# Performance work log

Measured on AMD Instinct MI355X. Metric: run time of the kernel, lower is better.

Reference implementation:

```python
import jax, jax.numpy as jnp
import numpy as np

DIM = 1024
NUM_HEADS = 16
HEAD_DIM = DIM // NUM_HEADS
SCALE = HEAD_DIM ** -0.5


def setup_inputs() -> dict:
    key = jax.random.key(0)
    ks = jax.random.split(key, 12)
    B, N, M, C = 4, 512, 2048, DIM
    x = jax.random.normal(ks[0], (B, N, C), dtype=jnp.float32)
    context = jax.random.normal(ks[1], (B, M, C), dtype=jnp.float32)
    mask = jax.random.randint(ks[2], (B, M), 0, 2, dtype=jnp.int32)
    mask = mask.at[:, 0].set(1)  # ensure at least one valid key per row
    w = 0.02
    Wq = jax.random.normal(ks[3], (C, C), dtype=jnp.float32) * w
    bq = jnp.zeros((C,), dtype=jnp.float32)
    Wk = jax.random.normal(ks[4], (C, C), dtype=jnp.float32) * w
    bk = jnp.zeros((C,), dtype=jnp.float32)
    Wv = jax.random.normal(ks[5], (C, C), dtype=jnp.float32) * w
    bv = jnp.zeros((C,), dtype=jnp.float32)
    Wo = jax.random.normal(ks[6], (C, C), dtype=jnp.float32) * w
    bo = jnp.zeros((C,), dtype=jnp.float32)
    return {"x": x, "context": context, "ctx_key_padding_mask": mask,
            "Wq": Wq, "bq": bq, "Wk": Wk, "bk": bk,
            "Wv": Wv, "bv": bv, "Wo": Wo, "bo": bo}


def reference(x, context, ctx_key_padding_mask, Wq, bq, Wk, bk, Wv, bv, Wo, bo):
    B, N, C = x.shape
    M = context.shape[1]
    H, D = NUM_HEADS, HEAD_DIM
    # torch nn.Linear: y = x @ W.T + b
    q = (x @ Wq.T + bq).reshape(B, N, H, D)
    k = (context @ Wk.T + bk).reshape(B, M, H, D)
    v = (context @ Wv.T + bv).reshape(B, M, H, D)
    scores = jnp.einsum('bnhd,bmhd->bhnm', q, k) * SCALE  # [B,H,N,M]
    neg = jnp.finfo(scores.dtype).min
    bias = jnp.where(ctx_key_padding_mask[:, None, None, :] != 0, 0.0, neg).astype(scores.dtype)
    attn = jax.nn.softmax(scores + bias, axis=-1)
    out = jnp.einsum('bhnm,bmhd->bnhd', attn, v).reshape(B, N, C)
    return out @ Wo.T + bo
```

## Files before the change

### kernel.cpp

```cpp
#include <hip/hip_runtime.h>
#include <hip/hip_bf16.h>
#include <stdint.h>


typedef __attribute__((ext_vector_type(4))) float f32x4;
typedef __attribute__((ext_vector_type(8))) __bf16 bf16x8;
typedef __attribute__((ext_vector_type(8))) unsigned short u16x8;

#define DEVI __device__ __forceinline__

#define QSC (0.125f * 1.44269504088896f)

DEVI f32x4 mfma16(u16x8 a, u16x8 b, f32x4 c) {
  return __builtin_amdgcn_mfma_f32_16x16x32_bf16(
      __builtin_bit_cast(bf16x8, a), __builtin_bit_cast(bf16x8, b), c, 0, 0, 0);
}

DEVI unsigned short f2bf(float f) {
  union { float f; unsigned int u; } x; x.f = f;
  unsigned int u = x.u;
  return (unsigned short)((u + 0x7fffu + ((u >> 16) & 1u)) >> 16);
}

DEVI float exp2_fast(float x) {
#if __has_builtin(__builtin_amdgcn_exp2f)
  return __builtin_amdgcn_exp2f(x);
#else
  return exp2f(x);
#endif
}

DEVI void llds16(const void* g, void* l) {
  __builtin_amdgcn_global_load_lds(
      (const __attribute__((address_space(1))) void*)g,
      (__attribute__((address_space(3))) void*)l, 16, 0, 0);
}

__global__ __launch_bounds__(256)
void cast_fused(const float* __restrict__ x, const float* __restrict__ ctx,
                const float* __restrict__ wq, const float* __restrict__ wk,
                const float* __restrict__ wv, const float* __restrict__ wo,
                unsigned short* __restrict__ xb, unsigned short* __restrict__ cb,
                unsigned short* __restrict__ wqb, unsigned short* __restrict__ wkb,
                unsigned short* __restrict__ wvb, unsigned short* __restrict__ wob) {
  int bid = blockIdx.x;
  const float* src; unsigned short* dst; float scale = 1.f;
  if (bid < 2048)        { src = x;   dst = xb; }
  else if (bid < 10240)  { src = ctx; dst = cb;  bid -= 2048; }
  else if (bid < 11264)  { src = wq;  dst = wqb; bid -= 10240; scale = QSC; }
  else if (bid < 12288)  { src = wk;  dst = wkb; bid -= 11264; }
  else if (bid < 13312)  { src = wv;  dst = wvb; bid -= 12288; }
  else                   { src = wo;  dst = wob; bid -= 13312; }
  int idx = (bid * 256 + threadIdx.x) * 4;
  const float4 v = *(const float4*)(src + idx);
  ushort4 o;
  o.x = f2bf(v.x * scale); o.y = f2bf(v.y * scale);
  o.z = f2bf(v.z * scale); o.w = f2bf(v.w * scale);
  *(ushort4*)(dst + idx) = o;
}

DEVI void epi_store(f32x4 (&acc)[4][4], const float* __restrict__ bias,
                    float bscale, void* __restrict__ Cout,
                    int bm, int bn, int logS, int mode,
                    unsigned short* cst, int tid, int wave, int l15, int quad) {
  const int wm = wave & 1, wn = wave >> 1;
  __syncthreads();
  for (int half = 0; half < 2; ++half) {
    if (wm == half) {
#pragma unroll
      for (int mi = 0; mi < 4; ++mi)
#pragma unroll
        for (int ni = 0; ni < 4; ++ni)
#pragma unroll
          for (int r = 0; r < 4; ++r) {
            int lrow = mi * 16 + quad * 4 + r;
            int lcol = wn * 64 + ni * 16 + l15;
            unsigned short bv = f2bf(acc[mi][ni][r] + bias[bn + lcol] * bscale);
            if (mode == 0) cst[lrow * 136 + lcol] = bv;
            else           cst[lcol * 72 + lrow] = bv;
          }
    }
    __syncthreads();
    if (mode == 0) {
      int lrow = tid >> 2, cc = (tid & 3) * 32;
      int row = bm + half * 64 + lrow;
      int S = 1 << logS;
      int b = row >> logS, sl = row & (S - 1);
#pragma unroll
      for (int j = 0; j < 4; ++j) {
        int col = bn + cc + j * 8;
        int h = col >> 6, d8 = (col & 63) >> 3;
        size_t base = (((size_t)(b * 16 + h)) << logS) * 64 +
                      (size_t)(sl >> 4) * 1024 + d8 * 128 + (sl & 15) * 8;
        *(u16x8*)&((unsigned short*)Cout)[base] =
            *(const u16x8*)&cst[lrow * 136 + cc + j * 8];
      }
    } else {
      int c = tid >> 1, rc = (tid & 1) * 32;
      int gc = bn + c, h = gc >> 6, d = gc & 63;
      int b = bm >> 11;
#pragma unroll
      for (int j = 0; j < 4; ++j) {
        int key = (bm & 2047) + half * 64 + rc + j * 8;
        size_t base = (size_t)(b * 16 + h) * 131072 +
                      (size_t)(((key >> 6) * 4 + (d >> 4)) * 8 + ((key >> 3) & 7)) * 128 +
                      (d & 15) * 8;
        *(u16x8*)&((unsigned short*)Cout)[base] =
            *(const u16x8*)&cst[c * 72 + rc + j * 8];
      }
    }
    __syncthreads();
  }
}

DEVI void kv_body(const unsigned short* __restrict__ A,
                  const unsigned short* __restrict__ WK,
                  const unsigned short* __restrict__ WV,
                  const float* __restrict__ bk, const float* __restrict__ bv,
                  unsigned short* __restrict__ kh, unsigned short* __restrict__ vt,
                  int bm, int bn, unsigned short* sh) {
  constexpr int K = 1024;
  unsigned short* As = sh;
  unsigned short* Ks = sh + 128 * 64;
  unsigned short* Vs = sh + 2 * 128 * 64;

  const int tid = threadIdx.x;
  const int wave = tid >> 6, lane = tid & 63;
  const int l15 = lane & 15, quad = lane >> 4;
  const int wm = wave & 1, wn = wave >> 1;

  f32x4 ak[4][4] = {}, av[4][4] = {};

  for (int k0 = 0; k0 < K; k0 += 64) {
    __syncthreads();
#pragma unroll
    for (int c = 0; c < 4; ++c) {
      int s = c * 256 + tid;
      int m = s >> 3;
      int k8 = (s & 7) ^ (m & 7);
      llds16(A + (size_t)(bm + m) * K + k0 + k8 * 8, &As[s * 8]);
      llds16(WK + (size_t)(bn + m) * K + k0 + k8 * 8, &Ks[s * 8]);
      llds16(WV + (size_t)(bn + m) * K + k0 + k8 * 8, &Vs[s * 8]);
    }
    __syncthreads();
#pragma unroll
    for (int ks = 0; ks < 2; ++ks) {
      const int k8 = ks * 4 + quad;
      u16x8 af[4], bf[4];
#pragma unroll
      for (int i = 0; i < 4; ++i) {
        int m = wm * 64 + i * 16 + l15;
        af[i] = *(const u16x8*)(&As[(m * 8 + (k8 ^ (m & 7))) * 8]);
      }
#pragma unroll
      for (int i = 0; i < 4; ++i) {
        int n = wn * 64 + i * 16 + l15;
        bf[i] = *(const u16x8*)(&Ks[(n * 8 + (k8 ^ (n & 7))) * 8]);
      }
#pragma unroll
      for (int mi = 0; mi < 4; ++mi)
#pragma unroll
        for (int ni = 0; ni < 4; ++ni)
          ak[mi][ni] = mfma16(af[mi], bf[ni], ak[mi][ni]);
#pragma unroll
      for (int i = 0; i < 4; ++i) {
        int n = wn * 64 + i * 16 + l15;
        bf[i] = *(const u16x8*)(&Vs[(n * 8 + (k8 ^ (n & 7))) * 8]);
      }
#pragma unroll
      for (int mi = 0; mi < 4; ++mi)
#pragma unroll
        for (int ni = 0; ni < 4; ++ni)
          av[mi][ni] = mfma16(af[mi], bf[ni], av[mi][ni]);
    }
  }

  epi_store(ak, bk, 1.f, kh, bm, bn, 11, 0, sh, tid, wave, l15, quad);
  epi_store(av, bv, 1.f, vt, bm, bn, 11, 2, sh, tid, wave, l15, quad);
}

DEVI void q_body(const unsigned short* __restrict__ A,
                 const unsigned short* __restrict__ W,
                 const float* __restrict__ bias,
                 unsigned short* __restrict__ Cout,
                 int bm, int bn, unsigned short* sh) {
  constexpr int K = 1024;
  unsigned short* As = sh;
  unsigned short* Bs = sh + 128 * 64;

  const int tid = threadIdx.x;
  const int wave = tid >> 6, lane = tid & 63;
  const int l15 = lane & 15, quad = lane >> 4;
  const int wm = wave & 1, wn = wave >> 1;

  f32x4 acc[4][4] = {};

  for (int k0 = 0; k0 < K; k0 += 64) {
    __syncthreads();
#pragma unroll
    for (int c = 0; c < 4; ++c) {
      int s = c * 256 + tid;
      int m = s >> 3;
      int k8 = (s & 7) ^ (m & 7);
      llds16(A + (size_t)(bm + m) * K + k0 + k8 * 8, &As[s * 8]);
      llds16(W + (size_t)(bn + m) * K + k0 + k8 * 8, &Bs[s * 8]);
    }
    __syncthreads();
#pragma unroll
    for (int ks = 0; ks < 2; ++ks) {
      const int k8 = ks * 4 + quad;
      u16x8 af[4], bf[4];
#pragma unroll
      for (int i = 0; i < 4; ++i) {
        int m = wm * 64 + i * 16 + l15;
        af[i] = *(const u16x8*)(&As[(m * 8 + (k8 ^ (m & 7))) * 8]);
        int n = wn * 64 + i * 16 + l15;
        bf[i] = *(const u16x8*)(&Bs[(n * 8 + (k8 ^ (n & 7))) * 8]);
      }
#pragma unroll
      for (int mi = 0; mi < 4; ++mi)
#pragma unroll
        for (int ni = 0; ni < 4; ++ni)
          acc[mi][ni] = mfma16(af[mi], bf[ni], acc[mi][ni]);
    }
  }

  epi_store(acc, bias, QSC, Cout, bm, bn, 9, 0, sh, tid, wave, l15, quad);
}

__global__ __launch_bounds__(256, 2)
void gemm_qkv(const unsigned short* __restrict__ xb,
              const unsigned short* __restrict__ cb,
              const unsigned short* __restrict__ wq,
              const unsigned short* __restrict__ wk,
              const unsigned short* __restrict__ wv,
              const float* __restrict__ bq, const float* __restrict__ bk,
              const float* __restrict__ bv,
              unsigned short* __restrict__ qh, unsigned short* __restrict__ kh,
              unsigned short* __restrict__ vt) {
  __shared__ __align__(16) unsigned short sh[128 * 64 * 3];
  const int x = blockIdx.x, y = blockIdx.y;
  if (y < 8) {
    kv_body(cb, wk, wv, bk, bv, kh, vt, x * 128, y * 128, sh);
  } else {
    q_body(xb, wq, bq, qh, (x & 15) * 128, (y - 8) * 512 + (x >> 4) * 128, sh);
  }
}

__global__ __launch_bounds__(256)
void gemm_o(const unsigned short* __restrict__ A,
            const unsigned short* __restrict__ W,
            const float* __restrict__ bo, float* __restrict__ out) {
  constexpr int K = 1024;
  __shared__ __align__(16) unsigned short As[64 * 64];
  __shared__ __align__(16) unsigned short Bs[128 * 64];

  const int tid = threadIdx.x;
  const int wave = tid >> 6, lane = tid & 63;
  const int l15 = lane & 15, quad = lane >> 4;
  const int bm = blockIdx.x * 64, bn = blockIdx.y * 128;

  f32x4 acc[4][2] = {};

  for (int k0 = 0; k0 < K; k0 += 64) {
    __syncthreads();
#pragma unroll
    for (int c = 0; c < 2; ++c) {
      int s = c * 256 + tid;
      int m = s >> 3, k8 = (s & 7) ^ (m & 7);
      llds16(A + (size_t)(bm + m) * K + k0 + k8 * 8, &As[s * 8]);
    }
#pragma unroll
    for (int c = 0; c < 4; ++c) {
      int s = c * 256 + tid;
      int m = s >> 3, k8 = (s & 7) ^ (m & 7);
      llds16(W + (size_t)(bn + m) * K + k0 + k8 * 8, &Bs[s * 8]);
    }
    __syncthreads();
#pragma unroll
    for (int ks = 0; ks < 2; ++ks) {
      const int k8 = ks * 4 + quad;
      u16x8 af[4], bf[2];
#pragma unroll
      for (int i = 0; i < 4; ++i) {
        int m = i * 16 + l15;
        af[i] = *(const u16x8*)(&As[(m * 8 + (k8 ^ (m & 7))) * 8]);
      }
#pragma unroll
      for (int i = 0; i < 2; ++i) {
        int n = wave * 32 + i * 16 + l15;
        bf[i] = *(const u16x8*)(&Bs[(n * 8 + (k8 ^ (n & 7))) * 8]);
      }
#pragma unroll
      for (int mi = 0; mi < 4; ++mi)
#pragma unroll
        for (int ni = 0; ni < 2; ++ni)
          acc[mi][ni] = mfma16(af[mi], bf[ni], acc[mi][ni]);
    }
  }

#pragma unroll
  for (int mi = 0; mi < 4; ++mi)
#pragma unroll
    for (int ni = 0; ni < 2; ++ni)
#pragma unroll
      for (int r = 0; r < 4; ++r) {
        int row = bm + mi * 16 + quad * 4 + r;
        int col = bn + wave * 32 + ni * 16 + l15;
        out[(size_t)row * 1024 + col] = acc[mi][ni][r] + bo[col];
      }
}

#define PS 72
__global__ __launch_bounds__(256, 1)
void attn_kernel(const unsigned short* __restrict__ Q,
                 const unsigned short* __restrict__ K,
                 const unsigned short* __restrict__ Vt,
                 const int* __restrict__ mask,
                 unsigned short* __restrict__ O) {
  __shared__ float bias_lds[2048];
  __shared__ __align__(16) unsigned short p_lds[4][2][16 * PS];
  __shared__ float l_lds[4][64];
  __shared__ __align__(16) float o_comb[64][68];

  const int tid = threadIdx.x;
  const int wave = tid >> 6, lane = tid & 63;
  const int l15 = lane & 15, quad = lane >> 4;
  const int bh = blockIdx.x, b = bh >> 4, h = bh & 15;
  const int q0 = blockIdx.y * 64;

  {
    const int* mb = mask + b * 2048;
    for (int i = tid; i < 2048; i += 256)
      bias_lds[i] = mb[i] ? -8.f : -1e30f;
  }
  __syncthreads();

  const unsigned short* Qb = Q + (size_t)bh * 32768 + (size_t)(q0 >> 4) * 1024;
  const unsigned short* Kb = K + (size_t)bh * 131072;
  const unsigned short* Vb = Vt + (size_t)bh * 131072;

  u16x8 aq[4][2];
#pragma unroll
  for (int qg = 0; qg < 4; ++qg)
#pragma unroll
    for (int ks = 0; ks < 2; ++ks)
      aq[qg][ks] = *(const u16x8*)(Qb + ((qg * 8 + ks * 4 + quad) * 16 + l15) * 8);

  f32x4 o_acc[4][4] = {};
  float l_s[4] = {0.f, 0.f, 0.f, 0.f};

  u16x8 kf[2][4];

  auto load_k = [&](int kb) {
    const int kg0 = kb >> 4;
#pragma unroll
    for (int ns = 0; ns < 4; ++ns)
#pragma unroll
      for (int ks = 0; ks < 2; ++ks)
        kf[ks][ns] = *(const u16x8*)(Kb + (((size_t)(kg0 + ns) * 8 + ks * 4 + quad) * 16 + l15) * 8);
  };

  load_k(wave * 64);

#pragma unroll 1
  for (int t = 0; t < 8; ++t) {
    const int kb = wave * 64 + t * 256;
    const int kb_next = kb + (t < 7 ? 256 : 0);

    u16x8 vf[2][4];
    const int kt4 = (kb >> 6) * 4;
#pragma unroll
    for (int nd = 0; nd < 4; ++nd)
#pragma unroll
      for (int ks = 0; ks < 2; ++ks)
        vf[ks][nd] = *(const u16x8*)(Vb + (((size_t)(kt4 + nd) * 8 + ks * 4 + quad) * 16 + l15) * 8);
    f32x4 bfr[4];
#pragma unroll
    for (int ns = 0; ns < 4; ++ns)
      bfr[ns] = *(const f32x4*)&bias_lds[kb + ns * 16 + quad * 4];

#pragma unroll
    for (int qg = 0; qg < 4; ++qg) {
      f32x4 sfr[4];
#pragma unroll
      for (int ns = 0; ns < 4; ++ns) {
        f32x4 sa = bfr[ns];
#pragma unroll
        for (int ks = 0; ks < 2; ++ks)
          sa = mfma16(kf[ks][ns], aq[qg][ks], sa);
        sfr[ns] = sa;
      }

      if (qg == 3) load_k(kb_next);

      float rsum = 0.f;
#pragma unroll
      for (int ns = 0; ns < 4; ++ns) {
        unsigned int pr[4];
#pragma unroll
        for (int r = 0; r < 4; ++r) {
          float p = exp2_fast(sfr[ns][r]);
          unsigned int u = __builtin_bit_cast(unsigned int, p) & 0xffff0000u;
          rsum += __builtin_bit_cast(float, u);
          pr[r] = u;
        }
        uint2 pw;
        pw.x = __builtin_amdgcn_perm(pr[1], pr[0], 0x07060302u);
        pw.y = __builtin_amdgcn_perm(pr[3], pr[2], 0x07060302u);
        *(uint2*)&p_lds[wave][qg & 1][l15 * PS + ns * 16 + quad * 4] = pw;
      }
      rsum += __shfl_xor(rsum, 16, 64);
      rsum += __shfl_xor(rsum, 32, 64);
      l_s[qg] += rsum;

#pragma unroll
      for (int ks = 0; ks < 2; ++ks) {
        u16x8 pf = *(const u16x8*)&p_lds[wave][qg & 1][l15 * PS + ks * 32 + quad * 8];
#pragma unroll
        for (int nd = 0; nd < 4; ++nd)
          o_acc[qg][nd] = mfma16(pf, vf[ks][nd], o_acc[qg][nd]);
      }
    }
  }

  if (quad == 0) {
#pragma unroll
    for (int qg = 0; qg < 4; ++qg)
      l_lds[wave][qg * 16 + l15] = l_s[qg];
  }
  __syncthreads();

  for (int w = 0; w < 4; ++w) {
    if (wave == w) {
#pragma unroll
      for (int qg = 0; qg < 4; ++qg)
#pragma unroll
        for (int r = 0; r < 4; ++r) {
          const int q = qg * 16 + quad * 4 + r;
#pragma unroll
          for (int nd = 0; nd < 4; ++nd) {
            const int d = nd * 16 + l15;
            float v = o_acc[qg][nd][r];
            if (w == 0) o_comb[q][d] = v;
            else        o_comb[q][d] += v;
          }
        }
    }
    __syncthreads();
  }

  {
    const int q = tid >> 2, dc = (tid & 3) * 16;
    const float inv = 1.f / (l_lds[0][q] + l_lds[1][q] + l_lds[2][q] + l_lds[3][q]);
    unsigned short* Ob = O + ((size_t)(b * 512 + q0 + q)) * 1024 + h * 64 + dc;
    u16x8 o1, o2;
#pragma unroll
    for (int j = 0; j < 8; ++j) o1[j] = f2bf(o_comb[q][dc + j] * inv);
#pragma unroll
    for (int j = 0; j < 8; ++j) o2[j] = f2bf(o_comb[q][dc + 8 + j] * inv);
    *(u16x8*)(Ob) = o1;
    *(u16x8*)(Ob + 8) = o2;
  }
}

extern "C" void kernel_launch(void* const* d_in, const int* in_sizes, int n_in,
                              void* d_out, int out_size, void* d_ws, size_t ws_size,
                              hipStream_t stream) {
  const float* x   = (const float*)d_in[0];
  const float* ctx = (const float*)d_in[1];
  const int* mask  = (const int*)d_in[2];
  const float* Wq  = (const float*)d_in[3];
  const float* bq  = (const float*)d_in[4];
  const float* Wk  = (const float*)d_in[5];
  const float* bk  = (const float*)d_in[6];
  const float* Wv  = (const float*)d_in[7];
  const float* bv  = (const float*)d_in[8];
  const float* Wo  = (const float*)d_in[9];
  const float* bo  = (const float*)d_in[10];

  char* ws = (char*)d_ws;
  unsigned short* xb  = (unsigned short*)(ws + ((size_t)0  << 20));
  unsigned short* cb  = (unsigned short*)(ws + ((size_t)4  << 20));
  unsigned short* wqb = (unsigned short*)(ws + ((size_t)20 << 20));
  unsigned short* wkb = (unsigned short*)(ws + ((size_t)22 << 20));
  unsigned short* wvb = (unsigned short*)(ws + ((size_t)24 << 20));
  unsigned short* wob = (unsigned short*)(ws + ((size_t)26 << 20));
  unsigned short* qh  = (unsigned short*)(ws + ((size_t)28 << 20));
  unsigned short* kh  = (unsigned short*)(ws + ((size_t)32 << 20));
  unsigned short* vt  = (unsigned short*)(ws + ((size_t)48 << 20));
  unsigned short* ah  = (unsigned short*)(ws + ((size_t)64 << 20));

  cast_fused<<<14336, 256, 0, stream>>>(x, ctx, Wq, Wk, Wv, Wo,
                                        xb, cb, wqb, wkb, wvb, wob);
  gemm_qkv<<<dim3(64, 10), 256, 0, stream>>>(xb, cb, wqb, wkb, wvb,
                                             bq, bk, bv, qh, kh, vt);
  attn_kernel<<<dim3(64, 8), 256, 0, stream>>>(qh, kh, vt, mask, ah);
  gemm_o<<<dim3(32, 8), 256, 0, stream>>>(ah, wob, bo, (float*)d_out);
}
```

Measured before the change: 212.0 us.

## Compact unmasked context rows and skip padded keys in KV projection and attention

After: 204.5 us. 1.04x faster.

```diff
diff --git a/kernel.cpp b/kernel.cpp
--- a/kernel.cpp
+++ b/kernel.cpp
@@ -37,26 +37,70 @@
 }
 
 __global__ __launch_bounds__(256)
+void compact_mask(const int* __restrict__ mask, int* __restrict__ cnt,
+                  int* __restrict__ idx) {
+  __shared__ int psum[256];
+  const int b = blockIdx.x, tid = threadIdx.x;
+  const int* mb = mask + b * 2048;
+  int v[8], s = 0;
+#pragma unroll
+  for (int j = 0; j < 8; ++j) { v[j] = (mb[tid * 8 + j] != 0); s += v[j]; }
+  psum[tid] = s;
+  __syncthreads();
+  for (int off = 1; off < 256; off <<= 1) {
+    int t = (tid >= off) ? psum[tid - off] : 0;
+    __syncthreads();
+    psum[tid] += t;
+    __syncthreads();
+  }
+  int base = tid ? psum[tid - 1] : 0;
+#pragma unroll
+  for (int j = 0; j < 8; ++j)
+    if (v[j]) { idx[b * 2048 + base] = tid * 8 + j; ++base; }
+  if (tid == 255) cnt[b] = psum[255];
+}
+
+__global__ __launch_bounds__(256)
 void cast_fused(const float* __restrict__ x, const float* __restrict__ ctx,
                 const float* __restrict__ wq, const float* __restrict__ wk,
                 const float* __restrict__ wv, const float* __restrict__ wo,
+                const int* __restrict__ cnt, const int* __restrict__ idx,
                 unsigned short* __restrict__ xb, unsigned short* __restrict__ cb,
                 unsigned short* __restrict__ wqb, unsigned short* __restrict__ wkb,
                 unsigned short* __restrict__ wvb, unsigned short* __restrict__ wob) {
   int bid = blockIdx.x;
+  const int tid = threadIdx.x;
+  if (bid >= 2048 && bid < 10240) {
+    int r = bid - 2048;
+    int b = r >> 11, j = r & 2047;
+    int c = cnt[b];
+    unsigned short* dst = cb + (size_t)r * 1024 + tid * 4;
+    if (j >= c) {
+      if (j < ((c + 255) & ~255)) {
+        ushort4 z; z.x = z.y = z.z = z.w = 0;
+        *(ushort4*)dst = z;
+      }
+      return;
+    }
+    const float* src = ctx + ((size_t)(b * 2048 + idx[b * 2048 + j])) * 1024 + tid * 4;
+    const float4 v = *(const float4*)src;
+    ushort4 o;
+    o.x = f2bf(v.x); o.y = f2bf(v.y); o.z = f2bf(v.z); o.w = f2bf(v.w);
+    *(ushort4*)dst = o;
+    return;
+  }
   const float* src; unsigned short* dst; float scale = 1.f;
   if (bid < 2048)        { src = x;   dst = xb; }
-  else if (bid < 10240)  { src = ctx; dst = cb;  bid -= 2048; }
   else if (bid < 11264)  { src = wq;  dst = wqb; bid -= 10240; scale = QSC; }
   else if (bid < 12288)  { src = wk;  dst = wkb; bid -= 11264; }
   else if (bid < 13312)  { src = wv;  dst = wvb; bid -= 12288; }
   else                   { src = wo;  dst = wob; bid -= 13312; }
-  int idx = (bid * 256 + threadIdx.x) * 4;
-  const float4 v = *(const float4*)(src + idx);
+  int e = (bid * 256 + tid) * 4;
+  const float4 v = *(const float4*)(src + e);
   ushort4 o;
   o.x = f2bf(v.x * scale); o.y = f2bf(v.y * scale);
   o.z = f2bf(v.z * scale); o.w = f2bf(v.w * scale);
-  *(ushort4*)(dst + idx) = o;
+  *(ushort4*)(dst + e) = o;
 }
 
 DEVI void epi_store(f32x4 (&acc)[4][4], const float* __restrict__ bias,
@@ -236,12 +280,16 @@
               const unsigned short* __restrict__ wv,
               const float* __restrict__ bq, const float* __restrict__ bk,
               const float* __restrict__ bv,
+              const int* __restrict__ cnt,
               unsigned short* __restrict__ qh, unsigned short* __restrict__ kh,
               unsigned short* __restrict__ vt) {
   __shared__ __align__(16) unsigned short sh[128 * 64 * 3];
   const int x = blockIdx.x, y = blockIdx.y;
   if (y < 8) {
-    kv_body(cb, wk, wv, bk, bv, kh, vt, x * 128, y * 128, sh);
+    const int bm = x * 128;
+    const int cpad = (cnt[bm >> 11] + 255) & ~255;
+    if ((bm & 2047) >= cpad) return;
+    kv_body(cb, wk, wv, bk, bv, kh, vt, bm, y * 128, sh);
   } else {
     q_body(xb, wq, bq, qh, (x & 15) * 128, (y - 8) * 512 + (x >> 4) * 128, sh);
   }
@@ -316,7 +364,7 @@
 void attn_kernel(const unsigned short* __restrict__ Q,
                  const unsigned short* __restrict__ K,
                  const unsigned short* __restrict__ Vt,
-                 const int* __restrict__ mask,
+                 const int* __restrict__ cnt,
                  unsigned short* __restrict__ O) {
   __shared__ float bias_lds[2048];
   __shared__ __align__(16) unsigned short p_lds[4][2][16 * PS];
@@ -329,11 +377,11 @@
   const int bh = blockIdx.x, b = bh >> 4, h = bh & 15;
   const int q0 = blockIdx.y * 64;
 
-  {
-    const int* mb = mask + b * 2048;
-    for (int i = tid; i < 2048; i += 256)
-      bias_lds[i] = mb[i] ? -8.f : -1e30f;
-  }
+  const int c = cnt[b];
+  const int T = (c + 255) >> 8;
+
+  for (int i = tid; i < 2048; i += 256)
+    bias_lds[i] = (i < c) ? -8.f : -1e30f;
   __syncthreads();
 
   const unsigned short* Qb = Q + (size_t)bh * 32768 + (size_t)(q0 >> 4) * 1024;
@@ -364,9 +412,9 @@
   load_k(wave * 64);
 
 #pragma unroll 1
-  for (int t = 0; t < 8; ++t) {
+  for (int t = 0; t < T; ++t) {
     const int kb = wave * 64 + t * 256;
-    const int kb_next = kb + (t < 7 ? 256 : 0);
+    const int kb_next = kb + (t + 1 < T ? 256 : 0);
 
     u16x8 vf[2][4];
     const int kt4 = (kb >> 6) * 4;
@@ -490,11 +538,14 @@
   unsigned short* kh  = (unsigned short*)(ws + ((size_t)32 << 20));
   unsigned short* vt  = (unsigned short*)(ws + ((size_t)48 << 20));
   unsigned short* ah  = (unsigned short*)(ws + ((size_t)64 << 20));
-
-  cast_fused<<<14336, 256, 0, stream>>>(x, ctx, Wq, Wk, Wv, Wo,
+  int* cnt = (int*)d_out;
+  int* idx = (int*)d_out + 4;
+
+  compact_mask<<<4, 256, 0, stream>>>(mask, cnt, idx);
+  cast_fused<<<14336, 256, 0, stream>>>(x, ctx, Wq, Wk, Wv, Wo, cnt, idx,
                                         xb, cb, wqb, wkb, wvb, wob);
   gemm_qkv<<<dim3(64, 10), 256, 0, stream>>>(xb, cb, wqb, wkb, wvb,
-                                             bq, bk, bv, qh, kh, vt);
-  attn_kernel<<<dim3(64, 8), 256, 0, stream>>>(qh, kh, vt, mask, ah);
+                                             bq, bk, bv, cnt, qh, kh, vt);
+  attn_kernel<<<dim3(64, 8), 256, 0, stream>>>(qh, kh, vt, cnt, ah);
   gemm_o<<<dim3(32, 8), 256, 0, stream>>>(ah, wob, bo, (float*)d_out);
 }
```

## Compact unmasked context rows and skip padded keys in KV projection and attention

Applied to the files above, without the earlier changes.

Result: faster. 190.5 us (-10.1%).

```diff
diff --git a/kernel.cpp b/kernel.cpp
--- a/kernel.cpp
+++ b/kernel.cpp
@@ -40,23 +40,64 @@
 void cast_fused(const float* __restrict__ x, const float* __restrict__ ctx,
                 const float* __restrict__ wq, const float* __restrict__ wk,
                 const float* __restrict__ wv, const float* __restrict__ wo,
+                const int* __restrict__ mask,
                 unsigned short* __restrict__ xb, unsigned short* __restrict__ cb,
                 unsigned short* __restrict__ wqb, unsigned short* __restrict__ wkb,
                 unsigned short* __restrict__ wvb, unsigned short* __restrict__ wob) {
   int bid = blockIdx.x;
+  const int tid = threadIdx.x;
+  if (bid >= 2048 && bid < 10240) {
+    __shared__ int red[256][2];
+    int r = bid - 2048;
+    int b = r >> 11, i = r & 2047;
+    const int* mb = mask + b * 2048;
+    int sall = 0, spre = 0;
+#pragma unroll
+    for (int j = 0; j < 8; ++j) {
+      int p = tid * 8 + j;
+      int v = (mb[p] != 0);
+      sall += v;
+      spre += (p < i) ? v : 0;
+    }
+    red[tid][0] = spre; red[tid][1] = sall;
+    __syncthreads();
+    for (int off = 128; off > 0; off >>= 1) {
+      if (tid < off) { red[tid][0] += red[tid + off][0]; red[tid][1] += red[tid + off][1]; }
+      __syncthreads();
+    }
+    const int pre = red[0][0], c = red[0][1];
+    const int valid = (mb[i] != 0);
+    int dst;
+    if (valid) {
+      dst = pre;
+    } else {
+      dst = c + (i - pre);
+      if (dst >= ((c + 255) & ~255)) return;
+    }
+    unsigned short* dp = cb + ((size_t)(b * 2048 + dst)) * 1024 + tid * 4;
+    if (valid) {
+      const float4 v = *(const float4*)(ctx + ((size_t)(b * 2048 + i)) * 1024 + tid * 4);
+      ushort4 o;
+      o.x = f2bf(v.x); o.y = f2bf(v.y); o.z = f2bf(v.z); o.w = f2bf(v.w);
+      *(ushort4*)dp = o;
+    } else {
+      ushort4 z; z.x = z.y = z.z = z.w = 0;
+      *(ushort4*)dp = z;
+    }
+    return;
+  }
   const float* src; unsigned short* dst; float scale = 1.f;
   if (bid < 2048)        { src = x;   dst = xb; }
-  else if (bid < 10240)  { src = ctx; dst = cb;  bid -= 2048; }
   else if (bid < 11264)  { src = wq;  dst = wqb; bid -= 10240; scale = QSC; }
   else if (bid < 12288)  { src = wk;  dst = wkb; bid -= 11264; }
   else if (bid < 13312)  { src = wv;  dst = wvb; bid -= 12288; }
   else                   { src = wo;  dst = wob; bid -= 13312; }
-  int idx = (bid * 256 + threadIdx.x) * 4;
-  const float4 v = *(const float4*)(src + idx);
+  int e = (bid * 256 + tid) * 4;
+  const float4 v = *(const float4*)(src + e);
   ushort4 o;
   o.x = f2bf(v.x * scale); o.y = f2bf(v.y * scale);
   o.z = f2bf(v.z * scale); o.w = f2bf(v.w * scale);
-  *(ushort4*)(dst + idx) = o;
+  *(ushort4*)(dst + e) = o;
 }
 
 DEVI void epi_store(f32x4 (&acc)[4][4], const float* __restrict__ bias,
@@ -236,14 +277,42 @@
               const unsigned short* __restrict__ wv,
               const float* __restrict__ bq, const float* __restrict__ bk,
               const float* __restrict__ bv,
+              const int* __restrict__ mask,
               unsigned short* __restrict__ qh, unsigned short* __restrict__ kh,
               unsigned short* __restrict__ vt) {
   __shared__ __align__(16) unsigned short sh[128 * 64 * 3];
-  const int x = blockIdx.x, y = blockIdx.y;
-  if (y < 8) {
-    kv_body(cb, wk, wv, bk, bv, kh, vt, x * 128, y * 128, sh);
-  } else {
-    q_body(xb, wq, bq, qh, (x & 15) * 128, (y - 8) * 512 + (x >> 4) * 128, sh);
+  __shared__ int qsum[260];
+  const int id = blockIdx.x;
+  const int tid = threadIdx.x;
+
+  {
+    int s = 0;
+    const int* mp = mask + tid * 32;
+#pragma unroll 8
+    for (int j = 0; j < 32; ++j) s += (mp[j] != 0);
+    qsum[tid] = s;
+    __syncthreads();
+    if (tid < 4) {
+      int tot = 0;
+      for (int k = 0; k < 64; ++k) tot += qsum[tid * 64 + k];
+      qsum[256 + tid] = tot;
+    }
+    __syncthreads();
+  }
+  const int nb0 = ((qsum[256] + 255) & ~255) >> 7;
+  const int nb1 = ((qsum[257] + 255) & ~255) >> 7;
+  const int nb2 = ((qsum[258] + 255) & ~255) >> 7;
+  const int nb3 = ((qsum[259] + 255) & ~255) >> 7;
+  const int L = nb0 + nb1 + nb2 + nb3;
+  if (id < L * 8) {
+    int xl = id >> 3, y = id & 7, b = 0;
+    if (xl >= nb0) { xl -= nb0; b = 1;
+      if (xl >= nb1) { xl -= nb1; b = 2;
+        if (xl >= nb2) { xl -= nb2; b = 3; } } }
+    kv_body(cb, wk, wv, bk, bv, kh, vt, b * 2048 + xl * 128, y * 128, sh);
+  } else if (id < L * 8 + 128) {
+    const int q = id - L * 8;
+    q_body(xb, wq, bq, qh, (q & 15) * 128, (q >> 4) * 128, sh);
   }
 }
 
@@ -312,16 +381,16 @@
 }
 
 #define PS 72
-__global__ __launch_bounds__(256, 1)
+__global__ __launch_bounds__(256, 2)
 void attn_kernel(const unsigned short* __restrict__ Q,
                  const unsigned short* __restrict__ K,
                  const unsigned short* __restrict__ Vt,
                  const int* __restrict__ mask,
                  unsigned short* __restrict__ O) {
-  __shared__ float bias_lds[2048];
   __shared__ __align__(16) unsigned short p_lds[4][2][16 * PS];
   __shared__ float l_lds[4][64];
   __shared__ __align__(16) float o_comb[64][68];
+  __shared__ int wsum[4];
 
   const int tid = threadIdx.x;
   const int wave = tid >> 6, lane = tid & 63;
@@ -331,10 +400,16 @@
 
   {
     const int* mb = mask + b * 2048;
-    for (int i = tid; i < 2048; i += 256)
-      bias_lds[i] = mb[i] ? -8.f : -1e30f;
-  }
-  __syncthreads();
+    int s = 0;
+#pragma unroll
+    for (int j = 0; j < 8; ++j) s += (mb[tid * 8 + j] != 0);
+#pragma unroll
+    for (int off = 1; off < 64; off <<= 1) s += __shfl_xor(s, off, 64);
+    if (lane == 0) wsum[wave] = s;
+    __syncthreads();
+  }
+  const int c = wsum[0] + wsum[1] + wsum[2] + wsum[3];
+  const int T = (c + 255) >> 8;
 
   const unsigned short* Qb = Q + (size_t)bh * 32768 + (size_t)(q0 >> 4) * 1024;
   const unsigned short* Kb = K + (size_t)bh * 131072;
@@ -364,9 +439,9 @@
   load_k(wave * 64);
 
 #pragma unroll 1
-  for (int t = 0; t < 8; ++t) {
+  for (int t = 0; t < T; ++t) {
     const int kb = wave * 64 + t * 256;
-    const int kb_next = kb + (t < 7 ? 256 : 0);
+    const int kb_next = kb + (t + 1 < T ? 256 : 0);
 
     u16x8 vf[2][4];
     const int kt4 = (kb >> 6) * 4;
@@ -375,10 +450,19 @@
 #pragma unroll
       for (int ks = 0; ks < 2; ++ks)
         vf[ks][nd] = *(const u16x8*)(Vb + (((size_t)(kt4 + nd) * 8 + ks * 4 + quad) * 16 + l15) * 8);
+
     f32x4 bfr[4];
-#pragma unroll
-    for (int ns = 0; ns < 4; ++ns)
-      bfr[ns] = *(const f32x4*)&bias_lds[kb + ns * 16 + quad * 4];
+    if (kb + 64 <= c) {
+#pragma unroll
+      for (int ns = 0; ns < 4; ++ns)
+        bfr[ns] = f32x4{-8.f, -8.f, -8.f, -8.f};
+    } else {
+#pragma unroll
+      for (int ns = 0; ns < 4; ++ns)
+#pragma unroll
+        for (int r = 0; r < 4; ++r)
+          bfr[ns][r] = (kb + ns * 16 + quad * 4 + r < c) ? -8.f : -1e30f;
+    }
 
 #pragma unroll
     for (int qg = 0; qg < 4; ++qg) {
@@ -491,10 +575,10 @@
   unsigned short* vt  = (unsigned short*)(ws + ((size_t)48 << 20));
   unsigned short* ah  = (unsigned short*)(ws + ((size_t)64 << 20));
 
-  cast_fused<<<14336, 256, 0, stream>>>(x, ctx, Wq, Wk, Wv, Wo,
+  cast_fused<<<14336, 256, 0, stream>>>(x, ctx, Wq, Wk, Wv, Wo, mask,
                                         xb, cb, wqb, wkb, wvb, wob);
-  gemm_qkv<<<dim3(64, 10), 256, 0, stream>>>(xb, cb, wqb, wkb, wvb,
-                                             bq, bk, bv, qh, kh, vt);
+  gemm_qkv<<<640, 256, 0, stream>>>(xb, cb, wqb, wkb, wvb,
+                                    bq, bk, bv, mask, qh, kh, vt);
   attn_kernel<<<dim3(64, 8), 256, 0, stream>>>(qh, kh, vt, mask, ah);
   gemm_o<<<dim3(32, 8), 256, 0, stream>>>(ah, wob, bo, (float*)d_out);
 }
```
